# Kernel optimization log

Hardware: AMD Instinct MI355X
Metric: run time of the kernel (lower is better)

The kernel has to match this reference:

```python
import jax, jax.numpy as jnp
import numpy as np

N_QUBITS = 4
N_LAYERS = 5
BOUNDS = jnp.array([4.8, 4.0, 0.418, 4.0], dtype=jnp.float32)

# sign of PauliZ eigenvalue for each of the 16 basis states, per qubit (wire 0 = MSB)
_Z_SIGNS = jnp.asarray(np.array([[1.0 if ((i >> (N_QUBITS - 1 - q)) & 1) == 0 else -1.0
                                  for q in range(N_QUBITS)] for i in range(2 ** N_QUBITS)],
                                 dtype=np.float32))


def _ry(theta):
    # RY(t) = [[cos t/2, -sin t/2], [sin t/2, cos t/2]]; theta (...,) -> (...,2,2) complex
    c = jnp.cos(theta / 2)
    s = jnp.sin(theta / 2)
    g = jnp.stack([jnp.stack([c, -s], -1), jnp.stack([s, c], -1)], -2)
    return g.astype(jnp.complex64)


def _rx(theta):
    # RX(t) = [[cos t/2, -i sin t/2], [-i sin t/2, cos t/2]]
    c = jnp.cos(theta / 2).astype(jnp.complex64)
    s = (-1j) * jnp.sin(theta / 2).astype(jnp.complex64)
    return jnp.stack([jnp.stack([c, s], -1), jnp.stack([s, c], -1)], -2)


def _apply_1q(state, gate, q):
    # state (B,2,2,2,2); gate (2,2) shared or (B,2,2) per-sample; wire q on axis q+1
    s = jnp.moveaxis(state, q + 1, 1)
    if gate.ndim == 3:
        s = jnp.einsum('bij,bj...->bi...', gate, s)
    else:
        s = jnp.einsum('ij,bj...->bi...', gate, s)
    return jnp.moveaxis(s, 1, q + 1)


def _cnot(state, c, t):
    # flip target axis on the control=1 slice
    s = jnp.moveaxis(state, (c + 1, t + 1), (1, 2))
    s = jnp.stack([s[:, 0], s[:, 1, ::-1]], axis=1)
    return jnp.moveaxis(s, (1, 2), (c + 1, t + 1))


def _forward(x, weights, W, b):
    B = x.shape[0]
    x_norm = jnp.clip(x / BOUNDS, -1.0, 1.0)
    angles = x_norm * jnp.pi                      # (B,4)
    ry = _ry(angles)                              # (B,4,2,2)
    state = jnp.zeros((B, 2, 2, 2, 2), jnp.complex64).at[:, 0, 0, 0, 0].set(1.0)
    for l in range(N_LAYERS):
        rx = _rx(weights[l])                      # (4,2,2)
        for q in range(N_QUBITS):                 # data re-uploading: AngleEmbedding RY
            state = _apply_1q(state, ry[:, q], q)
        for q in range(N_QUBITS):                 # BasicEntanglerLayers: RX rotations
            state = _apply_1q(state, rx[q], q)
        for q in range(N_QUBITS):                 # ring of CNOTs
            state = _cnot(state, q, (q + 1) % N_QUBITS)
    probs = (state.real ** 2 + state.imag ** 2).reshape(B, 2 ** N_QUBITS)
    feats = probs @ _Z_SIGNS                      # (B,4): <Z_q>
    return feats @ W.T + b                        # (B,2)


def setup_inputs() -> dict:
    key = jax.random.key(0)
    k1, k2, k3 = jax.random.split(key, 3)
    B = 524288
    x = jax.random.normal(k1, (B, 4), dtype=jnp.float32) * 2.0
    weights = jax.random.uniform(k2, (N_LAYERS, N_QUBITS), dtype=jnp.float32) * (2.0 * jnp.pi)
    W = jax.random.normal(k3, (2, 4), dtype=jnp.float32) * 0.5
    b = jnp.zeros((2,), dtype=jnp.float32)
    return {"x": x, "weights": weights, "W": W, "b": b}


def reference(x, weights, W, b):
    return _forward(x, weights, W, b)
```

## Files before the change

kernel.cpp:

```cpp
#include <hip/hip_runtime.h>


typedef float v2f __attribute__((ext_vector_type(2)));

__device__ __forceinline__ v2f splat(float x) { return (v2f){x, x}; }

__device__ __forceinline__ float rfl(float v) {
    return __uint_as_float(__builtin_amdgcn_readfirstlane(__float_as_uint(v)));
}

template<int MASK>
__device__ __forceinline__ void apply_ry(v2f (&re)[16], v2f (&im)[16], v2f c, v2f s) {
#pragma unroll
    for (int i0 = 0; i0 < 16; ++i0) {
        if (i0 & MASK) continue;
        const int i1 = i0 | MASK;
        v2f r0 = re[i0], r1 = re[i1];
        v2f m0 = im[i0], m1 = im[i1];
        re[i0] = c * r0 - s * r1;
        re[i1] = s * r0 + c * r1;
        im[i0] = c * m0 - s * m1;
        im[i1] = s * m0 + c * m1;
    }
}

template<int MASK>
__device__ __forceinline__ void apply_rx(v2f (&re)[16], v2f (&im)[16], v2f c, v2f s) {
#pragma unroll
    for (int i0 = 0; i0 < 16; ++i0) {
        if (i0 & MASK) continue;
        const int i1 = i0 | MASK;
        v2f r0 = re[i0], r1 = re[i1];
        v2f m0 = im[i0], m1 = im[i1];
        re[i0] = c * r0 + s * m1;
        im[i0] = c * m0 - s * r1;
        re[i1] = c * r1 + s * m0;
        im[i1] = c * m1 - s * r0;
    }
}

template<int CMASK, int TMASK>
__device__ __forceinline__ void apply_cnot(v2f (&re)[16], v2f (&im)[16]) {
#pragma unroll
    for (int i = 0; i < 16; ++i) {
        if ((i & CMASK) && !(i & TMASK)) {
            const int j = i | TMASK;
            v2f tr = re[i]; re[i] = re[j]; re[j] = tr;
            v2f ti = im[i]; im[i] = im[j]; im[j] = ti;
        }
    }
}

__global__ __launch_bounds__(256) void qdqn_kernel(
    const float* __restrict__ x,
    const float* __restrict__ weights,
    const float* __restrict__ Wm,
    const float* __restrict__ bv,
    float4* __restrict__ out,
    int Bh)
{
    float wc[20], ws[20], Wu[8];
    const float INV_4PI = 0.07957747154594767f;
#pragma unroll
    for (int k = 0; k < 20; ++k) {
        float rev = weights[k] * INV_4PI;
        wc[k] = rfl(__builtin_amdgcn_cosf(rev));
        ws[k] = rfl(__builtin_amdgcn_sinf(rev));
    }
#pragma unroll
    for (int k = 0; k < 8; ++k) Wu[k] = rfl(Wm[k]);
    const float b0u = rfl(bv[0]);
    const float b1u = rfl(bv[1]);

    const int t = blockIdx.x * blockDim.x + threadIdx.x;
    if (t >= Bh) return;

    const float4 xA = ((const float4*)x)[2 * t];
    const float4 xB = ((const float4*)x)[2 * t + 1];
    v2f xv[4] = { (v2f){xA.x, xB.x}, (v2f){xA.y, xB.y},
                  (v2f){xA.z, xB.z}, (v2f){xA.w, xB.w} };

    const float inv_bounds4[4] = { 0.25f / 4.8f, 0.25f / 4.0f, 0.25f / 0.418f, 0.25f / 4.0f };
    v2f rc[4], rs[4];
#pragma unroll
    for (int q = 0; q < 4; ++q) {
        v2f rev = xv[q] * splat(inv_bounds4[q]);
        float ra = fminf(fmaxf(rev.x, -0.25f), 0.25f);
        float rb = fminf(fmaxf(rev.y, -0.25f), 0.25f);
        rs[q] = (v2f){ __builtin_amdgcn_sinf(ra), __builtin_amdgcn_sinf(rb) };
        rc[q] = (v2f){ __builtin_amdgcn_cosf(ra), __builtin_amdgcn_cosf(rb) };
    }

    v2f ar[4], ai[4], br[4], bi[4];
#pragma unroll
    for (int q = 0; q < 4; ++q) {
        v2f cw = splat(wc[q]), sw = splat(ws[q]);
        ar[q] =  cw * rc[q];
        ai[q] = -sw * rs[q];
        br[q] =  cw * rs[q];
        bi[q] = -sw * rc[q];
    }
    v2f t2r[4], t2i[4];
#pragma unroll
    for (int i = 0; i < 4; ++i) {
        v2f xr = (i & 2) ? br[0] : ar[0], xi = (i & 2) ? bi[0] : ai[0];
        v2f yr = (i & 1) ? br[1] : ar[1], yi = (i & 1) ? bi[1] : ai[1];
        t2r[i] = xr * yr - xi * yi;
        t2i[i] = xr * yi + xi * yr;
    }
    v2f t3r[8], t3i[8];
#pragma unroll
    for (int i = 0; i < 8; ++i) {
        v2f xr = t2r[i >> 1], xi = t2i[i >> 1];
        v2f yr = (i & 1) ? br[2] : ar[2], yi = (i & 1) ? bi[2] : ai[2];
        t3r[i] = xr * yr - xi * yi;
        t3i[i] = xr * yi + xi * yr;
    }
    v2f re[16], im[16];
#pragma unroll
    for (int i = 0; i < 16; ++i) {
        v2f xr = t3r[i >> 1], xi = t3i[i >> 1];
        v2f yr = (i & 1) ? br[3] : ar[3], yi = (i & 1) ? bi[3] : ai[3];
        re[i] = xr * yr - xi * yi;
        im[i] = xr * yi + xi * yr;
    }
    apply_cnot<8, 4>(re, im);
    apply_cnot<4, 2>(re, im);
    apply_cnot<2, 1>(re, im);
    apply_cnot<1, 8>(re, im);

#pragma unroll
    for (int l = 1; l < 5; ++l) {
        apply_ry<8>(re, im, rc[0], rs[0]);
        apply_ry<4>(re, im, rc[1], rs[1]);
        apply_ry<2>(re, im, rc[2], rs[2]);
        apply_ry<1>(re, im, rc[3], rs[3]);
        apply_rx<8>(re, im, splat(wc[l * 4 + 0]), splat(ws[l * 4 + 0]));
        apply_rx<4>(re, im, splat(wc[l * 4 + 1]), splat(ws[l * 4 + 1]));
        apply_rx<2>(re, im, splat(wc[l * 4 + 2]), splat(ws[l * 4 + 2]));
        apply_rx<1>(re, im, splat(wc[l * 4 + 3]), splat(ws[l * 4 + 3]));
        apply_cnot<8, 4>(re, im);
        apply_cnot<4, 2>(re, im);
        apply_cnot<2, 1>(re, im);
        apply_cnot<1, 8>(re, im);
    }

    v2f p[16];
#pragma unroll
    for (int i = 0; i < 16; ++i) p[i] = re[i] * re[i] + im[i] * im[i];
    v2f tt[8];
#pragma unroll
    for (int i = 0; i < 8; ++i) tt[i] = p[2 * i] + p[2 * i + 1];
    v2f u[4];
#pragma unroll
    for (int i = 0; i < 4; ++i) u[i] = tt[2 * i] + tt[2 * i + 1];
    const v2f z0 = (u[0] + u[1]) - (u[2] + u[3]);
    const v2f z1 = (u[0] - u[1]) + (u[2] - u[3]);
    const v2f z2 = (tt[0] - tt[1]) + (tt[2] - tt[3])
                 + (tt[4] - tt[5]) + (tt[6] - tt[7]);
    const v2f z3 = ((p[0] - p[1]) + (p[2] - p[3]))
                 + ((p[4] - p[5]) + (p[6] - p[7]))
                 + ((p[8] - p[9]) + (p[10] - p[11]))
                 + ((p[12] - p[13]) + (p[14] - p[15]));

    v2f o0 = splat(b0u), o1 = splat(b1u);
    o0 = splat(Wu[0]) * z0 + o0; o0 = splat(Wu[1]) * z1 + o0;
    o0 = splat(Wu[2]) * z2 + o0; o0 = splat(Wu[3]) * z3 + o0;
    o1 = splat(Wu[4]) * z0 + o1; o1 = splat(Wu[5]) * z1 + o1;
    o1 = splat(Wu[6]) * z2 + o1; o1 = splat(Wu[7]) * z3 + o1;

    out[t] = make_float4(o0.x, o1.x, o0.y, o1.y);
}

extern "C" void kernel_launch(void* const* d_in, const int* in_sizes, int n_in,
                              void* d_out, int out_size, void* d_ws, size_t ws_size,
                              hipStream_t stream) {
    const float* x  = (const float*)d_in[0];
    const float* w  = (const float*)d_in[1];
    const float* Wm = (const float*)d_in[2];
    const float* bv = (const float*)d_in[3];
    float4* out = (float4*)d_out;

    const int B  = in_sizes[0] / 4;
    const int Bh = B / 2;
    dim3 grid((Bh + 255) / 256), block(256);
    qdqn_kernel<<<grid, block, 0, stream>>>(x, w, Wm, bv, out, Bh);
}
```

Before: 79.01 us.

## Switch state vector to packed fp16 and use three-shear rotations

The 16-amplitude complex state moves from packed fp32 to packed fp16 (h2), and each RY/RX rotation is rewritten as a three-shear form (x -= t*y; y += s*x; x -= t*y) with t = tan(theta/2), computed as s/(1+c). RX angles are wrapped so the tangent stays bounded. The goal is to halve the VALU work per gate via packed-half math and cut multiplies per pair from four to three. The cost is much lower precision through 20 gate layers, plus a conditioning risk for the shear form when the angle nears pi, which could break the accuracy tolerance.

```diff
diff --git a/kernel.cpp b/kernel.cpp
--- a/kernel.cpp
+++ b/kernel.cpp
@@ -1,52 +1,61 @@
 #include <hip/hip_runtime.h>
 
 
+typedef _Float16 h2 __attribute__((ext_vector_type(2)));
 typedef float v2f __attribute__((ext_vector_type(2)));
-
-__device__ __forceinline__ v2f splat(float x) { return (v2f){x, x}; }
 
 __device__ __forceinline__ float rfl(float v) {
     return __uint_as_float(__builtin_amdgcn_readfirstlane(__float_as_uint(v)));
 }
 
+__device__ __forceinline__ h2 usplat_h2(float v) {
+    _Float16 h = (_Float16)v;
+    unsigned short us = __builtin_bit_cast(unsigned short, h);
+    unsigned u = (unsigned)us | ((unsigned)us << 16);
+    u = __builtin_amdgcn_readfirstlane(u);
+    return __builtin_bit_cast(h2, u);
+}
+
 template<int MASK>
-__device__ __forceinline__ void apply_ry(v2f (&re)[16], v2f (&im)[16], v2f c, v2f s) {
+__device__ __forceinline__ void apply_ry_sh(h2 (&re)[16], h2 (&im)[16], h2 t, h2 s) {
 #pragma unroll
     for (int i0 = 0; i0 < 16; ++i0) {
         if (i0 & MASK) continue;
         const int i1 = i0 | MASK;
-        v2f r0 = re[i0], r1 = re[i1];
-        v2f m0 = im[i0], m1 = im[i1];
-        re[i0] = c * r0 - s * r1;
-        re[i1] = s * r0 + c * r1;
-        im[i0] = c * m0 - s * m1;
-        im[i1] = s * m0 + c * m1;
+        h2 x, y;
+        x = re[i0]; y = re[i1];
+        x = x - t * y; y = y + s * x; x = x - t * y;
+        re[i0] = x; re[i1] = y;
+        x = im[i0]; y = im[i1];
+        x = x - t * y; y = y + s * x; x = x - t * y;
+        im[i0] = x; im[i1] = y;
     }
 }
 
 template<int MASK>
-__device__ __forceinline__ void apply_rx(v2f (&re)[16], v2f (&im)[16], v2f c, v2f s) {
+__device__ __forceinline__ void apply_rx_sh(h2 (&re)[16], h2 (&im)[16], h2 t, h2 s) {
 #pragma unroll
     for (int i0 = 0; i0 < 16; ++i0) {
         if (i0 & MASK) continue;
         const int i1 = i0 | MASK;
-        v2f r0 = re[i0], r1 = re[i1];
-        v2f m0 = im[i0], m1 = im[i1];
-        re[i0] = c * r0 + s * m1;
-        im[i0] = c * m0 - s * r1;
-        re[i1] = c * r1 + s * m0;
-        im[i1] = c * m1 - s * r0;
+        h2 x, y;
+        x = re[i0]; y = im[i1];
+        x = x + t * y; y = y - s * x; x = x + t * y;
+        re[i0] = x; im[i1] = y;
+        x = im[i0]; y = re[i1];
+        x = x - t * y; y = y + s * x; x = x - t * y;
+        im[i0] = x; re[i1] = y;
     }
 }
 
 template<int CMASK, int TMASK>
-__device__ __forceinline__ void apply_cnot(v2f (&re)[16], v2f (&im)[16]) {
+__device__ __forceinline__ void apply_cnot(h2 (&re)[16], h2 (&im)[16]) {
 #pragma unroll
     for (int i = 0; i < 16; ++i) {
         if ((i & CMASK) && !(i & TMASK)) {
             const int j = i | TMASK;
-            v2f tr = re[i]; re[i] = re[j]; re[j] = tr;
-            v2f ti = im[i]; im[i] = im[j]; im[j] = ti;
+            h2 tr = re[i]; re[i] = re[j]; re[j] = tr;
+            h2 ti = im[i]; im[i] = im[j]; im[j] = ti;
         }
     }
 }
@@ -59,68 +68,82 @@
     float4* __restrict__ out,
     int Bh)
 {
-    float wc[20], ws[20], Wu[8];
     const float INV_4PI = 0.07957747154594767f;
+    float cw0[4], sw0[4];
+    h2 rxt[16], rxs[16];
 #pragma unroll
     for (int k = 0; k < 20; ++k) {
         float rev = weights[k] * INV_4PI;
-        wc[k] = rfl(__builtin_amdgcn_cosf(rev));
-        ws[k] = rfl(__builtin_amdgcn_sinf(rev));
-    }
+        if (k < 4) {
+            cw0[k] = rfl(__builtin_amdgcn_cosf(rev));
+            sw0[k] = rfl(__builtin_amdgcn_sinf(rev));
+        } else {
+            float r2 = (rev > 0.25f) ? (rev - 0.5f) : rev;
+            float c = __builtin_amdgcn_cosf(r2);
+            float s = __builtin_amdgcn_sinf(r2);
+            float t = s * __builtin_amdgcn_rcpf(1.0f + c);
+            rxt[k - 4] = usplat_h2(t);
+            rxs[k - 4] = usplat_h2(s);
+        }
+    }
+    float Wu[8];
 #pragma unroll
     for (int k = 0; k < 8; ++k) Wu[k] = rfl(Wm[k]);
     const float b0u = rfl(bv[0]);
     const float b1u = rfl(bv[1]);
 
-    const int t = blockIdx.x * blockDim.x + threadIdx.x;
-    if (t >= Bh) return;
-
-    const float4 xA = ((const float4*)x)[2 * t];
-    const float4 xB = ((const float4*)x)[2 * t + 1];
-    v2f xv[4] = { (v2f){xA.x, xB.x}, (v2f){xA.y, xB.y},
-                  (v2f){xA.z, xB.z}, (v2f){xA.w, xB.w} };
+    const int tid = blockIdx.x * blockDim.x + threadIdx.x;
+    if (tid >= Bh) return;
+
+    const float4 xA = ((const float4*)x)[2 * tid];
+    const float4 xB = ((const float4*)x)[2 * tid + 1];
+    float xvA[4] = { xA.x, xA.y, xA.z, xA.w };
+    float xvB[4] = { xB.x, xB.y, xB.z, xB.w };
 
     const float inv_bounds4[4] = { 0.25f / 4.8f, 0.25f / 4.0f, 0.25f / 0.418f, 0.25f / 4.0f };
-    v2f rc[4], rs[4];
+    float caA[4], saA[4], caB[4], saB[4];
+    h2 ryt[4], rys[4];
 #pragma unroll
     for (int q = 0; q < 4; ++q) {
-        v2f rev = xv[q] * splat(inv_bounds4[q]);
-        float ra = fminf(fmaxf(rev.x, -0.25f), 0.25f);
-        float rb = fminf(fmaxf(rev.y, -0.25f), 0.25f);
-        rs[q] = (v2f){ __builtin_amdgcn_sinf(ra), __builtin_amdgcn_sinf(rb) };
-        rc[q] = (v2f){ __builtin_amdgcn_cosf(ra), __builtin_amdgcn_cosf(rb) };
-    }
-
-    v2f ar[4], ai[4], br[4], bi[4];
+        float ra = fminf(fmaxf(xvA[q] * inv_bounds4[q], -0.25f), 0.25f);
+        float rb = fminf(fmaxf(xvB[q] * inv_bounds4[q], -0.25f), 0.25f);
+        saA[q] = __builtin_amdgcn_sinf(ra);  caA[q] = __builtin_amdgcn_cosf(ra);
+        saB[q] = __builtin_amdgcn_sinf(rb);  caB[q] = __builtin_amdgcn_cosf(rb);
+        float tA = saA[q] * __builtin_amdgcn_rcpf(1.0f + caA[q]);
+        float tB = saB[q] * __builtin_amdgcn_rcpf(1.0f + caB[q]);
+        ryt[q] = (h2){ (_Float16)tA, (_Float16)tB };
+        rys[q] = (h2){ (_Float16)saA[q], (_Float16)saB[q] };
+    }
+
+    h2 ar[4], ai[4], br[4], bi[4];
 #pragma unroll
     for (int q = 0; q < 4; ++q) {
-        v2f cw = splat(wc[q]), sw = splat(ws[q]);
-        ar[q] =  cw * rc[q];
-        ai[q] = -sw * rs[q];
-        br[q] =  cw * rs[q];
-        bi[q] = -sw * rc[q];
-    }
-    v2f t2r[4], t2i[4];
+        ar[q] = (h2){ (_Float16)( cw0[q] * caA[q]), (_Float16)( cw0[q] * caB[q]) };
+        ai[q] = (h2){ (_Float16)(-sw0[q] * saA[q]), (_Float16)(-sw0[q] * saB[q]) };
+        br[q] = (h2){ (_Float16)( cw0[q] * saA[q]), (_Float16)( cw0[q] * saB[q]) };
+        bi[q] = (h2){ (_Float16)(-sw0[q] * caA[q]), (_Float16)(-sw0[q] * caB[q]) };
+    }
+    h2 t2r[4], t2i[4];
 #pragma unroll
     for (int i = 0; i < 4; ++i) {
-        v2f xr = (i & 2) ? br[0] : ar[0], xi = (i & 2) ? bi[0] : ai[0];
-        v2f yr = (i & 1) ? br[1] : ar[1], yi = (i & 1) ? bi[1] : ai[1];
+        h2 xr = (i & 2) ? br[0] : ar[0], xi = (i & 2) ? bi[0] : ai[0];
+        h2 yr = (i & 1) ? br[1] : ar[1], yi = (i & 1) ? bi[1] : ai[1];
         t2r[i] = xr * yr - xi * yi;
         t2i[i] = xr * yi + xi * yr;
     }
-    v2f t3r[8], t3i[8];
+    h2 t3r[8], t3i[8];
 #pragma unroll
     for (int i = 0; i < 8; ++i) {
-        v2f xr = t2r[i >> 1], xi = t2i[i >> 1];
-        v2f yr = (i & 1) ? br[2] : ar[2], yi = (i & 1) ? bi[2] : ai[2];
+        h2 xr = t2r[i >> 1], xi = t2i[i >> 1];
+        h2 yr = (i & 1) ? br[2] : ar[2], yi = (i & 1) ? bi[2] : ai[2];
         t3r[i] = xr * yr - xi * yi;
         t3i[i] = xr * yi + xi * yr;
     }
-    v2f re[16], im[16];
+    h2 re[16], im[16];
 #pragma unroll
     for (int i = 0; i < 16; ++i) {
-        v2f xr = t3r[i >> 1], xi = t3i[i >> 1];
-        v2f yr = (i & 1) ? br[3] : ar[3], yi = (i & 1) ? bi[3] : ai[3];
+        h2 xr = t3r[i >> 1], xi = t3i[i >> 1];
+        h2 yr = (i & 1) ? br[3] : ar[3], yi = (i & 1) ? bi[3] : ai[3];
         re[i] = xr * yr - xi * yi;
         im[i] = xr * yi + xi * yr;
     }
@@ -131,14 +154,15 @@
 
 #pragma unroll
     for (int l = 1; l < 5; ++l) {
-        apply_ry<8>(re, im, rc[0], rs[0]);
-        apply_ry<4>(re, im, rc[1], rs[1]);
-        apply_ry<2>(re, im, rc[2], rs[2]);
-        apply_ry<1>(re, im, rc[3], rs[3]);
-        apply_rx<8>(re, im, splat(wc[l * 4 + 0]), splat(ws[l * 4 + 0]));
-        apply_rx<4>(re, im, splat(wc[l * 4 + 1]), splat(ws[l * 4 + 1]));
-        apply_rx<2>(re, im, splat(wc[l * 4 + 2]), splat(ws[l * 4 + 2]));
-        apply_rx<1>(re, im, splat(wc[l * 4 + 3]), splat(ws[l * 4 + 3]));
+        apply_ry_sh<8>(re, im, ryt[0], rys[0]);
+        apply_ry_sh<4>(re, im, ryt[1], rys[1]);
+        apply_ry_sh<2>(re, im, ryt[2], rys[2]);
+        apply_ry_sh<1>(re, im, ryt[3], rys[3]);
+        const int k = (l - 1) * 4;
+        apply_rx_sh<8>(re, im, rxt[k + 0], rxs[k + 0]);
+        apply_rx_sh<4>(re, im, rxt[k + 1], rxs[k + 1]);
+        apply_rx_sh<2>(re, im, rxt[k + 2], rxs[k + 2]);
+        apply_rx_sh<1>(re, im, rxt[k + 3], rxs[k + 3]);
         apply_cnot<8, 4>(re, im);
         apply_cnot<4, 2>(re, im);
         apply_cnot<2, 1>(re, im);
@@ -147,7 +171,10 @@
 
     v2f p[16];
 #pragma unroll
-    for (int i = 0; i < 16; ++i) p[i] = re[i] * re[i] + im[i] * im[i];
+    for (int i = 0; i < 16; ++i) {
+        h2 ph = re[i] * re[i] + im[i] * im[i];
+        p[i] = (v2f){ (float)ph.x, (float)ph.y };
+    }
     v2f tt[8];
 #pragma unroll
     for (int i = 0; i < 8; ++i) tt[i] = p[2 * i] + p[2 * i + 1];
@@ -163,13 +190,13 @@
                  + ((p[8] - p[9]) + (p[10] - p[11]))
                  + ((p[12] - p[13]) + (p[14] - p[15]));
 
-    v2f o0 = splat(b0u), o1 = splat(b1u);
-    o0 = splat(Wu[0]) * z0 + o0; o0 = splat(Wu[1]) * z1 + o0;
-    o0 = splat(Wu[2]) * z2 + o0; o0 = splat(Wu[3]) * z3 + o0;
-    o1 = splat(Wu[4]) * z0 + o1; o1 = splat(Wu[5]) * z1 + o1;
-    o1 = splat(Wu[6]) * z2 + o1; o1 = splat(Wu[7]) * z3 + o1;
-
-    out[t] = make_float4(o0.x, o1.x, o0.y, o1.y);
+    v2f o0 = (v2f){b0u, b0u}, o1 = (v2f){b1u, b1u};
+    o0 = (v2f){Wu[0], Wu[0]} * z0 + o0; o0 = (v2f){Wu[1], Wu[1]} * z1 + o0;
+    o0 = (v2f){Wu[2], Wu[2]} * z2 + o0; o0 = (v2f){Wu[3], Wu[3]} * z3 + o0;
+    o1 = (v2f){Wu[4], Wu[4]} * z0 + o1; o1 = (v2f){Wu[5], Wu[5]} * z1 + o1;
+    o1 = (v2f){Wu[6], Wu[6]} * z2 + o1; o1 = (v2f){Wu[7], Wu[7]} * z3 + o1;
+
+    out[tid] = make_float4(o0.x, o1.x, o0.y, o1.y);
 }
 
 extern "C" void kernel_launch(void* const* d_in, const int* in_sizes, int n_in,
```

After: 77.04 us. 1.03x faster.
